# Optimization experiments

Hardware: AMD Instinct MI355X
Metric: run time of the kernel (lower is better)

The kernel has to match this reference:

```python
import jax, jax.numpy as jnp
import numpy as np

DIM = 1024
N_HEADS = 16
HEAD_DIM = DIM // N_HEADS
MAX_SEQ = 2048
B, S = 4, 2048


def _rope_tables(seq_len):
    inv_freq = 1.0 / (10000.0 ** (jnp.arange(0, HEAD_DIM, 2, dtype=jnp.float32) / HEAD_DIM))
    t = jnp.arange(seq_len, dtype=jnp.float32)
    freqs = jnp.outer(t, inv_freq)            # [S, HEAD_DIM/2]
    emb = jnp.concatenate([freqs, freqs], -1)  # [S, HEAD_DIM]
    return jnp.cos(emb), jnp.sin(emb)


def _apply_rope(x, cos, sin):
    # x: [B, S, H, Dh]; cos/sin: [S, Dh]
    c = cos[None, :, None, :]
    s = sin[None, :, None, :]
    x1, x2 = jnp.split(x, 2, axis=-1)
    x_rot = jnp.concatenate([-x2, x1], -1)
    return x * c + x_rot * s


def setup_inputs() -> dict:
    key = jax.random.key(0)
    kx, kq, kk, kv, ko = jax.random.split(key, 5)
    std = DIM ** -0.5
    x = jax.random.normal(kx, (B, S, DIM), jnp.float32)
    Wq = jax.random.normal(kq, (DIM, DIM), jnp.float32) * std
    Wk = jax.random.normal(kk, (DIM, DIM), jnp.float32) * std
    Wv = jax.random.normal(kv, (DIM, DIM), jnp.float32) * std
    Wo = jax.random.normal(ko, (DIM, DIM), jnp.float32) * std
    # causal mask: 1 where attending is allowed, 0 where masked (mask==0 -> -inf)
    mask = jnp.tril(jnp.ones((S, S), jnp.int32))[None, None]  # [1,1,S,S]
    return {"x": x, "Wq": Wq, "Wk": Wk, "Wv": Wv, "Wo": Wo, "mask": mask}


def reference(x, Wq, Wk, Wv, Wo, mask) -> jnp.ndarray:
    b, s, _ = x.shape
    scale = HEAD_DIM ** -0.5
    # torch Linear: y = x @ W.T, W is [out, in]
    q = (x @ Wq.T).reshape(b, s, N_HEADS, HEAD_DIM)
    k = (x @ Wk.T).reshape(b, s, N_HEADS, HEAD_DIM)
    v = (x @ Wv.T).reshape(b, s, N_HEADS, HEAD_DIM)
    cos, sin = _rope_tables(s)
    q = _apply_rope(q, cos, sin)
    k = _apply_rope(k, cos, sin)
    # [B, H, S, S]
    attn = jnp.einsum('bqhd,bkhd->bhqk', q, k) * scale
    attn = jnp.where(mask == 0, -jnp.inf, attn)
    attn = jax.nn.softmax(attn, axis=-1)
    out = jnp.einsum('bhqk,bkhd->bqhd', attn, v).reshape(b, s, DIM)
    return out @ Wo.T
```

## Files before the change

### kernel.cpp

```cpp
#include <hip/hip_runtime.h>
#include <hip/hip_bf16.h>
#include <math.h>

using bf16 = __hip_bfloat16;
typedef __attribute__((ext_vector_type(8))) short short8;
typedef __attribute__((ext_vector_type(4))) float float4v;

#define DIM 1024
#define NH 16
#define HD 64
#define BB 4
#define SS 2048
#define MTOT (BB * SS)

#define ROPE_LOG2 0.41524101186092034f
#define PC1 0.18033688f
#define PC0 -23.08312066f

__device__ inline short bf16bits(float x) {
  return __builtin_bit_cast(short, __float2bfloat16(x));
}
__device__ inline float bits2f(unsigned short b) {
  return __builtin_bit_cast(float, (unsigned)b << 16);
}
__device__ inline unsigned pack2(float a, float b) {
  return (unsigned)(unsigned short)bf16bits(a) |
         ((unsigned)(unsigned short)bf16bits(b) << 16);
}

__device__ inline void async16(const void* g, void* l) {
  __builtin_amdgcn_global_load_lds(
      (const __attribute__((address_space(1))) void*)g,
      (__attribute__((address_space(3))) void*)l, 16, 0, 0);
}

__global__ __launch_bounds__(256) void rope_tab_k(unsigned* __restrict__ tab) {
  int i = blockIdx.x * 256 + threadIdx.x;
  int s = i >> 5, d = i & 31;
  float inv = exp2f(-(float)d * ROPE_LOG2);
  float sn, cs;
  sincosf((float)s * inv, &sn, &cs);
  tab[i] = pack2(cs, sn);
}

__device__ inline void cvt8(const float* __restrict__ in, bf16* __restrict__ out,
                            size_t i) {
  const float4v* p = (const float4v*)in + i * 2;
  float4v a = p[0], b = p[1];
  short8 r;
  r[0] = bf16bits(a[0]); r[1] = bf16bits(a[1]);
  r[2] = bf16bits(a[2]); r[3] = bf16bits(a[3]);
  r[4] = bf16bits(b[0]); r[5] = bf16bits(b[1]);
  r[6] = bf16bits(b[2]); r[7] = bf16bits(b[3]);
  ((short8*)out)[i] = r;
}

__global__ __launch_bounds__(256) void cvt_x(const float* __restrict__ in,
                                             bf16* __restrict__ out) {
  cvt8(in, out, (size_t)blockIdx.x * 256 + threadIdx.x);
}

__global__ __launch_bounds__(256) void cvt_w(const float* w0, const float* w1,
                                             const float* w2, const float* w3,
                                             bf16* o0, bf16* o1, bf16* o2,
                                             bf16* o3) {
  const float* in = blockIdx.y == 0 ? w0 : blockIdx.y == 1 ? w1
                    : blockIdx.y == 2 ? w2 : w3;
  bf16* out = blockIdx.y == 0 ? o0 : blockIdx.y == 1 ? o1
              : blockIdx.y == 2 ? o2 : o3;
  cvt8(in, out, (size_t)blockIdx.x * 256 + threadIdx.x);
}

__global__ __launch_bounds__(256, 2) void gemm_qkv(
    const bf16* __restrict__ A, const bf16* __restrict__ W,
    bf16* __restrict__ Cbase, const unsigned* __restrict__ rt) {
  __shared__ __align__(16) short sPool[8320];
  short* sA = sPool;
  short* sB = sPool + 4096;
  short* sT = sPool;

  const int tid = threadIdx.x;
  const int wave = tid >> 6;
  const int lane = tid & 63;
  const int l15 = lane & 15;
  const int quad = lane >> 4;
  const int m0 = blockIdx.x * 128;
  const int n0 = blockIdx.y * 128;
  const int wm = (wave >> 1) * 64;
  const int wn = (wave & 1) * 64;
  const int K = DIM;

  float4v acc[4][4];
#pragma unroll
  for (int i = 0; i < 4; i++)
#pragma unroll
    for (int j = 0; j < 4; j++)
#pragma unroll
      for (int r = 0; r < 4; r++) acc[i][j][r] = 0.0f;

  for (int k0 = 0; k0 < K; k0 += 32) {
    __syncthreads();
#pragma unroll
    for (int i = 0; i < 2; i++) {
      int c0 = i * 256 + wave * 64;
      int c = c0 + lane;
      int row = c >> 2, cb = c & 3;
      async16(A + (size_t)(m0 + row) * K + k0 + cb * 8, sA + c0 * 8);
      async16(W + (size_t)(n0 + row) * K + k0 + cb * 8, sB + c0 * 8);
    }
    __syncthreads();

    short8 af[4], bfr[4];
#pragma unroll
    for (int mi = 0; mi < 4; mi++)
      af[mi] = *(const short8*)(sA + (wm + mi * 16 + l15) * 32 + quad * 8);
#pragma unroll
    for (int ni = 0; ni < 4; ni++)
      bfr[ni] = *(const short8*)(sB + (wn + ni * 16 + l15) * 32 + quad * 8);
#pragma unroll
    for (int mi = 0; mi < 4; mi++)
#pragma unroll
      for (int ni = 0; ni < 4; ni++)
        acc[mi][ni] = __builtin_amdgcn_mfma_f32_16x16x32_bf16(
            af[mi], bfr[ni], acc[mi][ni], 0, 0, 0);
  }

  const int third = n0 >> 10;
  const int nloc = n0 & 1023;
  bf16* C = Cbase + (size_t)third * MTOT * DIM;

  if (third == 2) {
    const int bb_ = m0 >> 11;
    const int s0 = m0 & (SS - 1);
    const int h0 = nloc >> 6;
#pragma unroll
    for (int half = 0; half < 2; half++) {
      __syncthreads();
      if ((wave & 1) == half) {
#pragma unroll
        for (int mi = 0; mi < 4; mi++)
#pragma unroll
          for (int ni = 0; ni < 4; ni++)
#pragma unroll
            for (int r = 0; r < 4; r++)
              sT[(ni * 16 + l15) * 130 + wm + mi * 16 + quad * 4 + r] =
                  bf16bits(acc[mi][ni][r]);
      }
      __syncthreads();
      int row = tid >> 2, cb = tid & 3;
      size_t base =
          ((size_t)(bb_ * NH + h0 + half) * HD + row) * SS + s0 + cb * 32;
#pragma unroll
      for (int c = 0; c < 4; c++) {
        short8 vv = *(const short8*)(sT + row * 130 + cb * 32 + c * 8);
        *(short8*)((short*)C + base + c * 8) = vv;
      }
    }
    return;
  }

#pragma unroll
  for (int mi = 0; mi < 4; mi++) {
#pragma unroll
    for (int r = 0; r < 4; r++) {
      int m = m0 + wm + mi * 16 + quad * 4 + r;
      int b = m >> 11;
      int s = m & (SS - 1);
      int h = (nloc + wn) >> 6;
      bf16* outp = C + ((size_t)(b * NH + h) * SS + s) * HD;
#pragma unroll
      for (int ni = 0; ni < 2; ni++) {
        int d = ni * 16 + l15;
        unsigned cspack = rt[s * 32 + d];
        float cs = bits2f((unsigned short)(cspack & 0xffff));
        float sn = bits2f((unsigned short)(cspack >> 16));
        float lo = acc[mi][ni][r];
        float hi = acc[mi][ni + 2][r];
        outp[d] = __float2bfloat16(lo * cs - hi * sn);
        outp[d + 32] = __float2bfloat16(hi * cs + lo * sn);
      }
    }
  }
}

__global__ __launch_bounds__(256, 2) void gemm_out(const bf16* __restrict__ A,
                                                   const bf16* __restrict__ W,
                                                   float* __restrict__ C) {
  __shared__ __align__(16) short sA[128 * 32];
  __shared__ __align__(16) short sB[128 * 32];

  const int tid = threadIdx.x;
  const int wave = tid >> 6;
  const int lane = tid & 63;
  const int l15 = lane & 15;
  const int quad = lane >> 4;
  const int m0 = blockIdx.x * 128;
  const int n0 = blockIdx.y * 128;
  const int wm = (wave >> 1) * 64;
  const int wn = (wave & 1) * 64;
  const int K = DIM, N = DIM;

  float4v acc[4][4];
#pragma unroll
  for (int i = 0; i < 4; i++)
#pragma unroll
    for (int j = 0; j < 4; j++)
#pragma unroll
      for (int r = 0; r < 4; r++) acc[i][j][r] = 0.0f;

  for (int k0 = 0; k0 < K; k0 += 32) {
    __syncthreads();
#pragma unroll
    for (int i = 0; i < 2; i++) {
      int c0 = i * 256 + wave * 64;
      int c = c0 + lane;
      int row = c >> 2, cb = c & 3;
      async16(A + (size_t)(m0 + row) * K + k0 + cb * 8, sA + c0 * 8);
      async16(W + (size_t)(n0 + row) * K + k0 + cb * 8, sB + c0 * 8);
    }
    __syncthreads();

    short8 af[4], bfr[4];
#pragma unroll
    for (int mi = 0; mi < 4; mi++)
      af[mi] = *(const short8*)(sA + (wm + mi * 16 + l15) * 32 + quad * 8);
#pragma unroll
    for (int ni = 0; ni < 4; ni++)
      bfr[ni] = *(const short8*)(sB + (wn + ni * 16 + l15) * 32 + quad * 8);
#pragma unroll
    for (int mi = 0; mi < 4; mi++)
#pragma unroll
      for (int ni = 0; ni < 4; ni++)
        acc[mi][ni] = __builtin_amdgcn_mfma_f32_16x16x32_bf16(
            af[mi], bfr[ni], acc[mi][ni], 0, 0, 0);
  }

#pragma unroll
  for (int mi = 0; mi < 4; mi++) {
#pragma unroll
    for (int r = 0; r < 4; r++) {
      int m = m0 + wm + mi * 16 + quad * 4 + r;
#pragma unroll
      for (int ni = 0; ni < 4; ni++) {
        int n = n0 + wn + ni * 16 + l15;
        C[(size_t)m * N + n] = acc[mi][ni][r];
      }
    }
  }
}

#define SKV 64
#define SP 64

__global__ __launch_bounds__(256, 2) void attn_fwd(const bf16* __restrict__ q,
                                                   const bf16* __restrict__ k,
                                                   const bf16* __restrict__ vt,
                                                   bf16* __restrict__ o) {
  __shared__ __align__(16) short sK[2][64 * SKV];
  __shared__ __align__(16) short sV[2][64 * SKV];
  __shared__ __align__(16) short sP[4][16 * SP];

  const int tid = threadIdx.x;
  const int wave = tid >> 6;
  const int lane = tid & 63;
  const int l15 = lane & 15;
  const int quad = lane >> 4;
  const int bh = blockIdx.x;
  const int p = blockIdx.y;
  const int qt[4] = {p, 15 - p, 16 + p, 31 - p};
  const size_t hb = (size_t)bh * SS * HD;
  const size_t vtb = (size_t)bh * HD * SS;

  short8 aQ[4][2];
#pragma unroll
  for (int ti = 0; ti < 4; ti++) {
    const bf16* qp =
        q + hb + (size_t)(qt[ti] * 64 + wave * 16 + l15) * HD + quad * 8;
    aQ[ti][0] = *(const short8*)qp;
    aQ[ti][1] = *(const short8*)(qp + 32);
  }

  float l_part[4] = {0.0f, 0.0f, 0.0f, 0.0f};
  float4v acc_o[4][4];
#pragma unroll
  for (int ti = 0; ti < 4; ti++)
#pragma unroll
    for (int di = 0; di < 4; di++)
#pragma unroll
      for (int r = 0; r < 4; r++) acc_o[ti][di][r] = 0.0f;

  int4 kr[2], vr[2];
  auto load_kv = [&](int kt_) {
    int k0n = kt_ * 64;
#pragma unroll
    for (int i = 0; i < 2; i++) {
      int c = tid + i * 256;
      kr[i] = *(const int4*)(k + hb + (size_t)(k0n + (c >> 3)) * HD + (c & 7) * 8);
      vr[i] = *(const int4*)(vt + vtb + (size_t)(c >> 3) * SS + k0n + (c & 7) * 8);
    }
  };
  auto stage_write = [&](int buf) {
#pragma unroll
    for (int i = 0; i < 2; i++) {
      int c = tid + i * 256;
      int row = c >> 3;
      int sl = (c & 7) ^ (row & 7);
      *(int4*)(&sK[buf][row * SKV + sl * 8]) = kr[i];
      *(int4*)(&sV[buf][row * SKV + sl * 8]) = vr[i];
    }
  };

  load_kv(0);
  stage_write(0);
  __syncthreads();

  const int maxkt = qt[3];
  for (int kt = 0; kt <= maxkt; kt++) {
    const int cur = kt & 1;
    if (kt < maxkt) load_kv(kt + 1);

    short8 kf[8], vf[8];
#pragma unroll
    for (int t = 0; t < 2; t++)
#pragma unroll
      for (int i = 0; i < 4; i++) {
        int row = i * 16 + l15;
        int sl = (t * 4 + quad) ^ (l15 & 7);
        kf[t * 4 + i] = *(const short8*)(&sK[cur][row * SKV + sl * 8]);
        vf[t * 4 + i] = *(const short8*)(&sV[cur][row * SKV + sl * 8]);
      }

    const int k0 = kt * 64;
    short* pw = &sP[wave][0];
#pragma unroll
    for (int ti = 0; ti < 4; ti++) {
      if (kt <= qt[ti]) {
        float4v s[4];
#pragma unroll
        for (int ni = 0; ni < 4; ni++)
#pragma unroll
          for (int r = 0; r < 4; r++) s[ni][r] = 0.0f;
        __builtin_amdgcn_s_setprio(1);
#pragma unroll
        for (int t = 0; t < 2; t++)
#pragma unroll
          for (int ni = 0; ni < 4; ni++)
            s[ni] = __builtin_amdgcn_mfma_f32_16x16x32_bf16(
                kf[t * 4 + ni], aQ[ti][t], s[ni], 0, 0, 0);
        __builtin_amdgcn_s_setprio(0);

        const bool diag = (kt == qt[ti]);
        const int qglob = qt[ti] * 64 + wave * 16 + l15;
#pragma unroll
        for (int ni = 0; ni < 4; ni++) {
          float pe[4];
#pragma unroll
          for (int r = 0; r < 4; r++) {
            float x = exp2f(fmaf(s[ni][r], PC1, PC0));
            if (diag && (k0 + ni * 16 + quad * 4 + r > qglob)) x = 0.0f;
            l_part[ti] += x;
            pe[r] = x;
          }
          int2 w2;
          w2.x = (int)pack2(pe[0], pe[1]);
          w2.y = (int)pack2(pe[2], pe[3]);
          int slw = (2 * ni + (quad >> 1)) ^ (l15 & 7);
          *(int2*)(pw + l15 * SP + slw * 8 + (quad & 1) * 4) = w2;
        }
        asm volatile("s_waitcnt lgkmcnt(0)" ::: "memory");

        __builtin_amdgcn_s_setprio(1);
#pragma unroll
        for (int t = 0; t < 2; t++) {
          int slr = (t * 4 + quad) ^ (l15 & 7);
          short8 aP = *(const short8*)(pw + l15 * SP + slr * 8);
#pragma unroll
          for (int di = 0; di < 4; di++)
            acc_o[ti][di] = __builtin_amdgcn_mfma_f32_16x16x32_bf16(
                aP, vf[t * 4 + di], acc_o[ti][di], 0, 0, 0);
        }
        __builtin_amdgcn_s_setprio(0);
      }
    }

    if (kt < maxkt) stage_write(cur ^ 1);
    __syncthreads();
  }

  const int b = bh >> 4, h = bh & 15;
#pragma unroll
  for (int ti = 0; ti < 4; ti++) {
    float lr = l_part[ti];
    lr += __shfl_xor(lr, 16, 64);
    lr += __shfl_xor(lr, 32, 64);
#pragma unroll
    for (int r = 0; r < 4; r++) {
      float invl = 1.0f / __shfl(lr, quad * 4 + r, 64);
      bf16* op =
          o + (size_t)(b * SS + qt[ti] * 64 + wave * 16 + quad * 4 + r) * DIM +
          h * HD;
#pragma unroll
      for (int di = 0; di < 4; di++)
        op[di * 16 + l15] = __float2bfloat16(acc_o[ti][di][r] * invl);
    }
  }
}

extern "C" void kernel_launch(void* const* d_in, const int* in_sizes, int n_in,
                              void* d_out, int out_size, void* d_ws,
                              size_t ws_size, hipStream_t stream) {
  const float* x = (const float*)d_in[0];
  const float* Wq = (const float*)d_in[1];
  const float* Wk = (const float*)d_in[2];
  const float* Wv = (const float*)d_in[3];
  const float* Wo = (const float*)d_in[4];
  float* out = (float*)d_out;

  char* ws = (char*)d_ws;
  const size_t xsz = (size_t)MTOT * DIM * sizeof(bf16);
  bf16* xb = (bf16*)ws;
  bf16* qb_ = (bf16*)(ws + xsz);
  bf16* kb = (bf16*)(ws + 2 * xsz);
  bf16* vtb = (bf16*)(ws + 3 * xsz);
  bf16* wqb = (bf16*)(ws + 4 * xsz);
  bf16* wkb = wqb + (size_t)DIM * DIM;
  bf16* wvb = wkb + (size_t)DIM * DIM;
  bf16* wob = wvb + (size_t)DIM * DIM;
  unsigned* rt = (unsigned*)(wob + (size_t)DIM * DIM);
  bf16* ob = xb;

  dim3 bb(256);
  rope_tab_k<<<dim3(SS * 32 / 256), bb, 0, stream>>>(rt);
  cvt_x<<<dim3(MTOT * DIM / 8 / 256), bb, 0, stream>>>(x, xb);
  cvt_w<<<dim3(DIM * DIM / 8 / 256, 4), bb, 0, stream>>>(Wq, Wk, Wv, Wo, wqb,
                                                         wkb, wvb, wob);
  gemm_qkv<<<dim3(MTOT / 128, 3 * DIM / 128), bb, 0, stream>>>(xb, wqb, qb_,
                                                               rt);
  attn_fwd<<<dim3(BB * NH, 8), bb, 0, stream>>>(qb_, kb, vtb, ob);
  gemm_out<<<dim3(MTOT / 128, DIM / 128), bb, 0, stream>>>(ob, wob, out);
}
```

Measured before the change: 301.4 us.

## Double-buffer LDS tiles in QKV and output GEMMs to overlap loads with MFMA

Both projection GEMMs move from a single shared-memory tile to two ping-pong buffers. The next K-slice is issued asynchronously before computing on the current one, leaving one barrier per iteration instead of two. The occupancy hint in launch bounds rises from 2 to 3 blocks per CU. This doubles LDS per block and depends on the async loads being complete at the trailing barrier; the higher occupancy target may also constrain registers and cause spills.

```diff
diff --git a/kernel.cpp b/kernel.cpp
--- a/kernel.cpp
+++ b/kernel.cpp
@@ -71,13 +71,11 @@
   cvt8(in, out, (size_t)blockIdx.x * 256 + threadIdx.x);
 }
 
-__global__ __launch_bounds__(256, 2) void gemm_qkv(
+__global__ __launch_bounds__(256, 3) void gemm_qkv(
     const bf16* __restrict__ A, const bf16* __restrict__ W,
     bf16* __restrict__ Cbase, const unsigned* __restrict__ rt) {
-  __shared__ __align__(16) short sPool[8320];
-  short* sA = sPool;
-  short* sB = sPool + 4096;
-  short* sT = sPool;
+  __shared__ __align__(16) short sPool[4][4096];
+  short* sT = &sPool[0][0];
 
   const int tid = threadIdx.x;
   const int wave = tid >> 6;
@@ -98,18 +96,28 @@
 #pragma unroll
       for (int r = 0; r < 4; r++) acc[i][j][r] = 0.0f;
 
-  for (int k0 = 0; k0 < K; k0 += 32) {
-    __syncthreads();
+  auto stage = [&](int buf, int k0) {
+    short* dA = &sPool[buf * 2][0];
+    short* dB = &sPool[buf * 2 + 1][0];
 #pragma unroll
     for (int i = 0; i < 2; i++) {
       int c0 = i * 256 + wave * 64;
       int c = c0 + lane;
       int row = c >> 2, cb = c & 3;
-      async16(A + (size_t)(m0 + row) * K + k0 + cb * 8, sA + c0 * 8);
-      async16(W + (size_t)(n0 + row) * K + k0 + cb * 8, sB + c0 * 8);
-    }
-    __syncthreads();
-
+      async16(A + (size_t)(m0 + row) * K + k0 + cb * 8, dA + c0 * 8);
+      async16(W + (size_t)(n0 + row) * K + k0 + cb * 8, dB + c0 * 8);
+    }
+  };
+
+  stage(0, 0);
+  __syncthreads();
+
+  int cur = 0;
+  for (int k0 = 0; k0 < K; k0 += 32, cur ^= 1) {
+    if (k0 + 32 < K) stage(cur ^ 1, k0 + 32);
+
+    const short* sA = &sPool[cur * 2][0];
+    const short* sB = &sPool[cur * 2 + 1][0];
     short8 af[4], bfr[4];
 #pragma unroll
     for (int mi = 0; mi < 4; mi++)
@@ -123,6 +131,8 @@
       for (int ni = 0; ni < 4; ni++)
         acc[mi][ni] = __builtin_amdgcn_mfma_f32_16x16x32_bf16(
             af[mi], bfr[ni], acc[mi][ni], 0, 0, 0);
+
+    __syncthreads();
   }
 
   const int third = n0 >> 10;
@@ -135,7 +145,7 @@
     const int h0 = nloc >> 6;
 #pragma unroll
     for (int half = 0; half < 2; half++) {
-      __syncthreads();
+      if (half) __syncthreads();
       if ((wave & 1) == half) {
 #pragma unroll
         for (int mi = 0; mi < 4; mi++)
@@ -183,11 +193,10 @@
   }
 }
 
-__global__ __launch_bounds__(256, 2) void gemm_out(const bf16* __restrict__ A,
+__global__ __launch_bounds__(256, 3) void gemm_out(const bf16* __restrict__ A,
                                                    const bf16* __restrict__ W,
                                                    float* __restrict__ C) {
-  __shared__ __align__(16) short sA[128 * 32];
-  __shared__ __align__(16) short sB[128 * 32];
+  __shared__ __align__(16) short sPool[4][4096];
 
   const int tid = threadIdx.x;
   const int wave = tid >> 6;
@@ -208,18 +217,28 @@
 #pragma unroll
       for (int r = 0; r < 4; r++) acc[i][j][r] = 0.0f;
 
-  for (int k0 = 0; k0 < K; k0 += 32) {
-    __syncthreads();
+  auto stage = [&](int buf, int k0) {
+    short* dA = &sPool[buf * 2][0];
+    short* dB = &sPool[buf * 2 + 1][0];
 #pragma unroll
     for (int i = 0; i < 2; i++) {
       int c0 = i * 256 + wave * 64;
       int c = c0 + lane;
       int row = c >> 2, cb = c & 3;
-      async16(A + (size_t)(m0 + row) * K + k0 + cb * 8, sA + c0 * 8);
-      async16(W + (size_t)(n0 + row) * K + k0 + cb * 8, sB + c0 * 8);
-    }
-    __syncthreads();
-
+      async16(A + (size_t)(m0 + row) * K + k0 + cb * 8, dA + c0 * 8);
+      async16(W + (size_t)(n0 + row) * K + k0 + cb * 8, dB + c0 * 8);
+    }
+  };
+
+  stage(0, 0);
+  __syncthreads();
+
+  int cur = 0;
+  for (int k0 = 0; k0 < K; k0 += 32, cur ^= 1) {
+    if (k0 + 32 < K) stage(cur ^ 1, k0 + 32);
+
+    const short* sA = &sPool[cur * 2][0];
+    const short* sB = &sPool[cur * 2 + 1][0];
     short8 af[4], bfr[4];
 #pragma unroll
     for (int mi = 0; mi < 4; mi++)
@@ -233,6 +252,8 @@
       for (int ni = 0; ni < 4; ni++)
         acc[mi][ni] = __builtin_amdgcn_mfma_f32_16x16x32_bf16(
             af[mi], bfr[ni], acc[mi][ni], 0, 0, 0);
+
+    __syncthreads();
   }
 
 #pragma unroll
```

After: 292.5 us. -2.9%, faster.

## Triple-buffer GEMM K-loop with async LDS prefetch and XOR-swizzled tiles

Applied to the files above, without the earlier changes.

Replaces the single-buffered load-then-compute K loop in both projection GEMMs with a three-stage ring of LDS buffers. Tiles two steps ahead are prefetched with global_load_lds while MFMAs run, and a waitcnt+barrier replaces the two __syncthreads per step. The tile columns are also XOR-swizzled to reduce LDS bank conflicts, MFMA issue priority is raised, and the launch bound is increased to 3 blocks per CU. LDS per block grows to 48KB, which may limit occupancy. The inline-asm vmcnt accounting also relies on each stage issuing exactly four loads per thread.

```diff
diff --git a/kernel.cpp b/kernel.cpp
--- a/kernel.cpp
+++ b/kernel.cpp
@@ -12,6 +12,7 @@
 #define BB 4
 #define SS 2048
 #define MTOT (BB * SS)
+#define NKT (DIM / 32)
 
 #define ROPE_LOG2 0.41524101186092034f
 #define PC1 0.18033688f
@@ -71,13 +72,53 @@
   cvt8(in, out, (size_t)blockIdx.x * 256 + threadIdx.x);
 }
 
-__global__ __launch_bounds__(256, 2) void gemm_qkv(
+#define GEMM_STAGE(buf, k0)                                               \
+  {                                                                       \
+    short* dA = &sPool[(buf) * 2][0];                                     \
+    short* dB = &sPool[(buf) * 2 + 1][0];                                 \
+    _Pragma("unroll") for (int i = 0; i < 2; i++) {                       \
+      int c0 = i * 256 + wave * 64;                                       \
+      int c = c0 + lane;                                                  \
+      int row = c >> 2;                                                   \
+      int cb = (c & 3) ^ ((c >> 3) & 3);   \
+      async16(A + (size_t)(m0 + row) * DIM + (k0) + cb * 8, dA + c0 * 8); \
+      async16(W + (size_t)(n0 + row) * DIM + (k0) + cb * 8, dB + c0 * 8); \
+    }                                                                     \
+  }
+
+#define GEMM_KLOOP()                                                         \
+  GEMM_STAGE(0, 0);                                                          \
+  GEMM_STAGE(1, 32);                                                         \
+  asm volatile("s_waitcnt vmcnt(4)\ns_barrier" ::: "memory");                \
+  for (int kt = 0; kt < NKT; kt++) {                                         \
+    if (kt + 2 < NKT) GEMM_STAGE((kt + 2) % 3, (kt + 2) * 32);               \
+    const short* sA = &sPool[(kt % 3) * 2][0];                               \
+    const short* sB = &sPool[(kt % 3) * 2 + 1][0];                           \
+    const int sw = (l15 >> 1) & 3;                                           \
+    short8 af[4], bfr[4];                                                    \
+    _Pragma("unroll") for (int mi = 0; mi < 4; mi++) af[mi] =                \
+        *(const short8*)(sA + (wm + mi * 16 + l15) * 32 + (quad ^ sw) * 8);  \
+    _Pragma("unroll") for (int ni = 0; ni < 4; ni++) bfr[ni] =               \
+        *(const short8*)(sB + (wn + ni * 16 + l15) * 32 + (quad ^ sw) * 8);  \
+    __builtin_amdgcn_s_setprio(1);                                           \
+    _Pragma("unroll") for (int mi = 0; mi < 4; mi++)                         \
+        _Pragma("unroll") for (int ni = 0; ni < 4; ni++) acc[mi][ni] =       \
+            __builtin_amdgcn_mfma_f32_16x16x32_bf16(af[mi], bfr[ni],         \
+                                                    acc[mi][ni], 0, 0, 0);   \
+    __builtin_amdgcn_s_setprio(0);                                           \
+    if (kt < NKT - 1) {                                                      \
+      if (kt + 2 < NKT)                                                      \
+        asm volatile("s_waitcnt vmcnt(4)\ns_barrier" ::: "memory");          \
+      else                                                                   \
+        asm volatile("s_waitcnt vmcnt(0)\ns_barrier" ::: "memory");          \
+    }                                                                        \
+  }
+
+__global__ __launch_bounds__(256, 3) void gemm_qkv(
     const bf16* __restrict__ A, const bf16* __restrict__ W,
     bf16* __restrict__ Cbase, const unsigned* __restrict__ rt) {
-  __shared__ __align__(16) short sPool[8320];
-  short* sA = sPool;
-  short* sB = sPool + 4096;
-  short* sT = sPool;
+  __shared__ __align__(16) short sPool[6][4096];
+  short* sT = &sPool[0][0];
 
   const int tid = threadIdx.x;
   const int wave = tid >> 6;
@@ -88,7 +129,6 @@
   const int n0 = blockIdx.y * 128;
   const int wm = (wave >> 1) * 64;
   const int wn = (wave & 1) * 64;
-  const int K = DIM;
 
   float4v acc[4][4];
 #pragma unroll
@@ -98,32 +138,7 @@
 #pragma unroll
       for (int r = 0; r < 4; r++) acc[i][j][r] = 0.0f;
 
-  for (int k0 = 0; k0 < K; k0 += 32) {
-    __syncthreads();
-#pragma unroll
-    for (int i = 0; i < 2; i++) {
-      int c0 = i * 256 + wave * 64;
-      int c = c0 + lane;
-      int row = c >> 2, cb = c & 3;
-      async16(A + (size_t)(m0 + row) * K + k0 + cb * 8, sA + c0 * 8);
-      async16(W + (size_t)(n0 + row) * K + k0 + cb * 8, sB + c0 * 8);
-    }
-    __syncthreads();
-
-    short8 af[4], bfr[4];
-#pragma unroll
-    for (int mi = 0; mi < 4; mi++)
-      af[mi] = *(const short8*)(sA + (wm + mi * 16 + l15) * 32 + quad * 8);
-#pragma unroll
-    for (int ni = 0; ni < 4; ni++)
-      bfr[ni] = *(const short8*)(sB + (wn + ni * 16 + l15) * 32 + quad * 8);
-#pragma unroll
-    for (int mi = 0; mi < 4; mi++)
-#pragma unroll
-      for (int ni = 0; ni < 4; ni++)
-        acc[mi][ni] = __builtin_amdgcn_mfma_f32_16x16x32_bf16(
-            af[mi], bfr[ni], acc[mi][ni], 0, 0, 0);
-  }
+  GEMM_KLOOP();
 
   const int third = n0 >> 10;
   const int nloc = n0 & 1023;
@@ -183,11 +198,10 @@
   }
 }
 
-__global__ __launch_bounds__(256, 2) void gemm_out(const bf16* __restrict__ A,
+__global__ __launch_bounds__(256, 3) void gemm_out(const bf16* __restrict__ A,
                                                    const bf16* __restrict__ W,
                                                    float* __restrict__ C) {
-  __shared__ __align__(16) short sA[128 * 32];
-  __shared__ __align__(16) short sB[128 * 32];
+  __shared__ __align__(16) short sPool[6][4096];
 
   const int tid = threadIdx.x;
   const int wave = tid >> 6;
@@ -198,7 +212,7 @@
   const int n0 = blockIdx.y * 128;
   const int wm = (wave >> 1) * 64;
   const int wn = (wave & 1) * 64;
-  const int K = DIM, N = DIM;
+  const int N = DIM;
 
   float4v acc[4][4];
 #pragma unroll
@@ -208,32 +222,7 @@
 #pragma unroll
       for (int r = 0; r < 4; r++) acc[i][j][r] = 0.0f;
 
-  for (int k0 = 0; k0 < K; k0 += 32) {
-    __syncthreads();
-#pragma unroll
-    for (int i = 0; i < 2; i++) {
-      int c0 = i * 256 + wave * 64;
-      int c = c0 + lane;
-      int row = c >> 2, cb = c & 3;
-      async16(A + (size_t)(m0 + row) * K + k0 + cb * 8, sA + c0 * 8);
-      async16(W + (size_t)(n0 + row) * K + k0 + cb * 8, sB + c0 * 8);
-    }
-    __syncthreads();
-
-    short8 af[4], bfr[4];
-#pragma unroll
-    for (int mi = 0; mi < 4; mi++)
-      af[mi] = *(const short8*)(sA + (wm + mi * 16 + l15) * 32 + quad * 8);
-#pragma unroll
-    for (int ni = 0; ni < 4; ni++)
-      bfr[ni] = *(const short8*)(sB + (wn + ni * 16 + l15) * 32 + quad * 8);
-#pragma unroll
-    for (int mi = 0; mi < 4; mi++)
-#pragma unroll
-      for (int ni = 0; ni < 4; ni++)
-        acc[mi][ni] = __builtin_amdgcn_mfma_f32_16x16x32_bf16(
-            af[mi], bfr[ni], acc[mi][ni], 0, 0, 0);
-  }
+  GEMM_KLOOP();
 
 #pragma unroll
   for (int mi = 0; mi < 4; mi++) {
```

Measured after the change: 298.7 us. About the same (-0.9%).
